# Performance work log

Hardware: AMD Instinct MI355X
Metric: run time of the kernel (lower is better)

## Reference

```python
import jax, jax.numpy as jnp
import numpy as np

E, TOPK, H, I, NSH = 8, 2, 2048, 5120, 2
B, S = 2, 1024


def setup_inputs() -> dict:
    key = jax.random.key(0)
    ks = jax.random.split(key, 8)
    sc = 0.02
    return {
        "x": jax.random.normal(ks[0], (B, S, H), dtype=jnp.float32),
        "w_router": jax.random.normal(ks[1], (E, H), dtype=jnp.float32),
        "wg": jax.random.normal(ks[2], (E, I, H), dtype=jnp.float32) * sc,
        "wu": jax.random.normal(ks[3], (E, I, H), dtype=jnp.float32) * sc,
        "wd": jax.random.normal(ks[4], (E, H, I), dtype=jnp.float32) * sc,
        "sg": jax.random.normal(ks[5], (NSH, I, H), dtype=jnp.float32) * sc,
        "su": jax.random.normal(ks[6], (NSH, I, H), dtype=jnp.float32) * sc,
        "sd": jax.random.normal(ks[7], (NSH, H, I), dtype=jnp.float32) * sc,
    }


def reference(x, w_router, wg, wu, wd, sg, su, sd):
    b, s, h = x.shape
    xt = x.reshape(-1, h)  # [T, H]
    T = xt.shape[0]

    # Router: fp32 linear, sigmoid scores, top-k, renormalize
    logits = jnp.einsum('th,eh->te', xt.astype(jnp.float32), w_router.astype(jnp.float32))
    scores = jax.nn.sigmoid(logits)
    topk_w, topk_i = jax.lax.top_k(scores, TOPK)
    topk_w = topk_w / jnp.sum(topk_w, axis=-1, keepdims=True)

    # Dense combine weights [T, E]: zero for non-selected experts
    comb = jnp.zeros((T, E), dtype=xt.dtype)
    comb = comb.at[jnp.arange(T)[:, None], topk_i].add(topk_w.astype(xt.dtype))

    # Routed experts (SwiGLU, no bias): compute all, combine with sparse weights
    gate = jax.nn.silu(jnp.einsum('th,eih->tei', xt, wg))
    up = jnp.einsum('th,eih->tei', xt, wu)
    expert_out = jnp.einsum('tei,ehi->teh', gate * up, wd)
    out = jnp.einsum('te,teh->th', comb, expert_out)

    # Shared experts: applied to every token, summed
    sgate = jax.nn.silu(jnp.einsum('th,jih->tji', xt, sg))
    sup = jnp.einsum('th,jih->tji', xt, su)
    out = out + jnp.einsum('tji,jhi->th', sgate * sup, sd)

    return out.reshape(b, s, h)
```

## Files before the change

kernel.cpp:

```cpp
#include <hip/hip_runtime.h>
#include <stdint.h>


#define E_ 8
#define H_ 2048
#define I_ 5120
#define T_ 2048
#define NSLOT 10

typedef __attribute__((ext_vector_type(4))) float f32x4;
typedef __attribute__((ext_vector_type(8))) __bf16 bf16x8;
typedef __attribute__((ext_vector_type(4))) unsigned int u32x4;
typedef __attribute__((ext_vector_type(2))) unsigned int u32x2;

__device__ __forceinline__ int sw(int r) { return (r ^ (r >> 2)) & 3; }

__device__ __forceinline__ unsigned short f2bf(float f) {
  unsigned u = __builtin_bit_cast(unsigned, f);
  u += 0x7FFFu + ((u >> 16) & 1u);
  return (unsigned short)(u >> 16);
}

__device__ __forceinline__ u32x2 cvt4(f32x4 v) {
  unsigned r0, r1;
  asm("v_cvt_pk_bf16_f32 %0, %1, %2" : "=v"(r0) : "v"(v[0]), "v"(v[1]));
  asm("v_cvt_pk_bf16_f32 %0, %1, %2" : "=v"(r1) : "v"(v[2]), "v"(v[3]));
  u32x2 w; w[0] = r0; w[1] = r1;
  return w;
}

__global__ __launch_bounds__(256) void k_castx(const float* __restrict__ x,
                                               unsigned short* __restrict__ xb) {
  const int i = (blockIdx.x * 256 + threadIdx.x) * 8;
  f32x4 a = *(const f32x4*)(x + i);
  f32x4 b = *(const f32x4*)(x + i + 4);
  u32x2 lo = cvt4(a), hi = cvt4(b);
  u32x4 o; o[0] = lo[0]; o[1] = lo[1]; o[2] = hi[0]; o[3] = hi[1];
  *(u32x4*)(xb + i) = o;
}

__global__ __launch_bounds__(64) void k_router(const float* __restrict__ x,
                                               const float* __restrict__ wr,
                                               int* __restrict__ tki,
                                               float* __restrict__ tkw) {
  const int t = blockIdx.x, lane = threadIdx.x;
  const float* xr = x + (size_t)t * H_;
  float lg[E_];
#pragma unroll
  for (int e = 0; e < E_; ++e) {
    const float* w = wr + (size_t)e * H_;
    float acc = 0.f;
    for (int k = lane; k < H_; k += 64) acc += xr[k] * w[k];
#pragma unroll
    for (int off = 32; off > 0; off >>= 1) acc += __shfl_down(acc, off);
    lg[e] = acc;
  }
  if (lane == 0) {
    float sc[E_];
#pragma unroll
    for (int e = 0; e < E_; ++e) sc[e] = 1.f / (1.f + expf(-lg[e]));
    int b0 = 0;
#pragma unroll
    for (int e = 1; e < E_; ++e) if (sc[e] > sc[b0]) b0 = e;
    int b1 = -1;
#pragma unroll
    for (int e = 0; e < E_; ++e) {
      if (e == b0) continue;
      if (b1 < 0 || sc[e] > sc[b1]) b1 = e;
    }
    float s0 = sc[b0], s1 = sc[b1], inv = 1.f / (s0 + s1);
    tki[2 * t] = b0; tki[2 * t + 1] = b1;
    tkw[2 * t] = s0 * inv; tkw[2 * t + 1] = s1 * inv;
  }
}

__global__ __launch_bounds__(64) void k_lists(const int* __restrict__ tki,
                                              const float* __restrict__ tkw,
                                              int* __restrict__ elist,
                                              float* __restrict__ ew,
                                              int* __restrict__ ecnt,
                                              int* __restrict__ ipos) {
  const int s = blockIdx.x, lane = threadIdx.x;
  if (s < E_) {
    int base = 0;
    for (int c = 0; c < T_ / 64; ++c) {
      int t = c * 64 + lane;
      int i0 = tki[2 * t], i1 = tki[2 * t + 1];
      int flag = (i0 == s) ? 1 : ((i1 == s) ? 2 : 0);
      unsigned long long m = __ballot(flag != 0);
      int pre = __popcll(m & ((1ull << lane) - 1ull));
      if (flag) {
        elist[s * T_ + base + pre] = t;
        ew[s * T_ + base + pre] = tkw[2 * t + flag - 1];
        ipos[2 * t + flag - 1] = base + pre;
      }
      base += __popcll(m);
    }
    int padded = (base + 255) & ~255;
    for (int p = base + lane; p < padded; p += 64) { elist[s * T_ + p] = 0; ew[s * T_ + p] = 0.f; }
    if (lane == 0) ecnt[s] = base;
  } else {
    for (int i = lane; i < T_; i += 64) { elist[s * T_ + i] = i; ew[s * T_ + i] = 1.f; }
    if (lane == 0) ecnt[s] = T_;
  }
}

__global__ void k_bases(const int* __restrict__ ecnt, int* __restrict__ sbase) {
  if (threadIdx.x == 0 && blockIdx.x == 0) {
    int b = 0;
    for (int s = 0; s < NSLOT; ++s) { sbase[s] = b; b += (ecnt[s] + 255) & ~255; }
  }
}

__global__ __launch_bounds__(1024, 4) void k_gateup(
    const unsigned short* __restrict__ xb,
    const float* __restrict__ wg_all, const float* __restrict__ wu_all,
    const float* __restrict__ sg_all, const float* __restrict__ su_all,
    const int* __restrict__ elist, const float* __restrict__ ew,
    const int* __restrict__ ecnt,
    const int* __restrict__ sbase, unsigned short* __restrict__ h) {
  const int s = blockIdx.z;
  const int cnt = ecnt[s];
  const int r0 = blockIdx.y * 256;
  if (r0 >= cnt) return;
  const int n0 = blockIdx.x * 128;
  const float* gw; const float* uw;
  if (s < E_) { gw = wg_all + (size_t)s * I_ * H_; uw = wu_all + (size_t)s * I_ * H_; }
  else        { gw = sg_all + (size_t)(s - E_) * I_ * H_; uw = su_all + (size_t)(s - E_) * I_ * H_; }
  const int* lst = elist + s * T_;
  const int hrow0 = sbase[s] + r0;

  __shared__ u32x4 sA[2][256 * 4];
  __shared__ u32x4 sG[2][128 * 4];
  __shared__ u32x4 sU[2][128 * 4];

  const int tid = threadIdx.x;
  const int w = tid >> 6, lane = tid & 63;
  const int wr = w >> 2, wc = w & 3;
  const int fr = lane & 15, k8 = lane >> 4;

  const int ar = tid >> 2, ca = tid & 3;
  int li = r0 + ar; if (li >= cnt) li = r0;
  const unsigned short* xp = xb + (size_t)lst[li] * H_ + ca * 8;
  const int br = tid >> 3, cb = (tid & 7) >> 1, bh = tid & 1;
  const float* gp = gw + (size_t)(n0 + br) * H_ + (tid & 7) * 4;
  const float* up = uw + (size_t)(n0 + br) * H_ + (tid & 7) * 4;

  u32x4 ra; f32x4 rg, ru;

  f32x4 accg[4][2], accu[4][2];
#pragma unroll
  for (int m = 0; m < 4; ++m)
#pragma unroll
    for (int n = 0; n < 2; ++n) {
      accg[m][n] = (f32x4){0.f, 0.f, 0.f, 0.f};
      accu[m][n] = (f32x4){0.f, 0.f, 0.f, 0.f};
    }

  auto loadNext = [&]() {
    ra = *(const u32x4*)xp; rg = *(const f32x4*)gp; ru = *(const f32x4*)up;
    xp += 32; gp += 32; up += 32;
  };
  auto stage = [&](int b) {
    sA[b][ar * 4 + (ca ^ sw(ar))] = ra;
    ((u32x2*)&sG[b][br * 4 + (cb ^ sw(br))])[bh] = cvt4(rg);
    ((u32x2*)&sU[b][br * 4 + (cb ^ sw(br))])[bh] = cvt4(ru);
  };
  auto compute = [&](int b) {
    bf16x8 af[4], gf[2], uf[2];
#pragma unroll
    for (int m = 0; m < 4; ++m) {
      int r = wr * 64 + m * 16 + fr;
      af[m] = __builtin_bit_cast(bf16x8, sA[b][r * 4 + (k8 ^ sw(r))]);
    }
#pragma unroll
    for (int n = 0; n < 2; ++n) {
      int r = wc * 32 + n * 16 + fr;
      gf[n] = __builtin_bit_cast(bf16x8, sG[b][r * 4 + (k8 ^ sw(r))]);
      uf[n] = __builtin_bit_cast(bf16x8, sU[b][r * 4 + (k8 ^ sw(r))]);
    }
#pragma unroll
    for (int m = 0; m < 4; ++m)
#pragma unroll
      for (int n = 0; n < 2; ++n) {
        accg[m][n] = __builtin_amdgcn_mfma_f32_16x16x32_bf16(af[m], gf[n], accg[m][n], 0, 0, 0);
        accu[m][n] = __builtin_amdgcn_mfma_f32_16x16x32_bf16(af[m], uf[n], accu[m][n], 0, 0, 0);
      }
  };

  const int KT = H_ / 32;
  loadNext();
  stage(0);
  loadNext();
  __syncthreads();
  int cur = 0;
  for (int kt = 0; kt < KT; ++kt) {
    compute(cur);
    if (kt + 1 < KT) {
      stage(cur ^ 1);
      if (kt + 2 < KT) loadNext();
      __syncthreads();
      cur ^= 1;
    }
  }

#pragma unroll
  for (int m = 0; m < 4; ++m)
#pragma unroll
    for (int r = 0; r < 4; ++r) {
      int rit = wr * 64 + m * 16 + k8 * 4 + r;
      if (r0 + rit < cnt) {
        float wgt = ew[s * T_ + r0 + rit];
        unsigned short* hrow = h + (size_t)(hrow0 + rit) * I_ + n0 + wc * 32;
#pragma unroll
        for (int n = 0; n < 2; ++n) {
          float g = accg[m][n][r], uv = accu[m][n][r];
          float hv = g / (1.f + expf(-g)) * uv * wgt;
          hrow[n * 16 + fr] = f2bf(hv);
        }
      }
    }
}

__global__ __launch_bounds__(512, 4) void k_down(
    const unsigned short* __restrict__ h,
    const float* __restrict__ wd_all, const float* __restrict__ sd_all,
    const int* __restrict__ elist,
    const int* __restrict__ ecnt, const int* __restrict__ sbase,
    float* __restrict__ y, int use_y,
    float* __restrict__ out) {
  const int s = blockIdx.z;
  const int cnt = ecnt[s];
  const int r0 = blockIdx.y * 256;
  if (r0 >= cnt) return;
  const int n0 = blockIdx.x * 128;
  const float* bw = (s < E_) ? wd_all + (size_t)s * H_ * I_
                             : sd_all + (size_t)(s - E_) * H_ * I_;
  const int hrow0 = sbase[s] + r0;

  __shared__ u32x4 sA[2][256 * 4];
  __shared__ u32x4 sB[2][128 * 4];

  const int tid = threadIdx.x;
  const int wv = tid >> 6, lane = tid & 63;
  const int wr = wv >> 1, wc = wv & 1;
  const int fr = lane & 15, k8 = lane >> 4;

  const int ar = tid >> 1, ca2 = (tid & 1) * 2;
  const unsigned short* hp = h + (size_t)(hrow0 + ar) * I_ + ca2 * 8;
  const int brr = tid >> 2, cb = tid & 3;
  const float* bp = bw + (size_t)(n0 + brr) * I_ + cb * 8;

  u32x4 ra0, ra1; f32x4 rb0, rb1;

  f32x4 acc[4][4];
#pragma unroll
  for (int m = 0; m < 4; ++m)
#pragma unroll
    for (int n = 0; n < 4; ++n) acc[m][n] = (f32x4){0.f, 0.f, 0.f, 0.f};

  auto loadNext = [&]() {
    ra0 = *(const u32x4*)hp; ra1 = *(const u32x4*)(hp + 8); hp += 32;
    rb0 = *(const f32x4*)bp; rb1 = *(const f32x4*)(bp + 4); bp += 32;
  };
  auto stage = [&](int b) {
    sA[b][ar * 4 + (ca2 ^ sw(ar))] = ra0;
    sA[b][ar * 4 + ((ca2 + 1) ^ sw(ar))] = ra1;
    u32x2 lo = cvt4(rb0), hi = cvt4(rb1);
    u32x4 q; q[0] = lo[0]; q[1] = lo[1]; q[2] = hi[0]; q[3] = hi[1];
    sB[b][brr * 4 + (cb ^ sw(brr))] = q;
  };
  auto compute = [&](int b) {
    bf16x8 af[4], bf[4];
#pragma unroll
    for (int m = 0; m < 4; ++m) {
      int r = wr * 64 + m * 16 + fr;
      af[m] = __builtin_bit_cast(bf16x8, sA[b][r * 4 + (k8 ^ sw(r))]);
    }
#pragma unroll
    for (int n = 0; n < 4; ++n) {
      int r = wc * 64 + n * 16 + fr;
      bf[n] = __builtin_bit_cast(bf16x8, sB[b][r * 4 + (k8 ^ sw(r))]);
    }
#pragma unroll
    for (int m = 0; m < 4; ++m)
#pragma unroll
      for (int n = 0; n < 4; ++n)
        acc[m][n] = __builtin_amdgcn_mfma_f32_16x16x32_bf16(af[m], bf[n], acc[m][n], 0, 0, 0);
  };

  const int KT = I_ / 32;
  loadNext();
  stage(0);
  loadNext();
  __syncthreads();
  int cur = 0;
  for (int kt = 0; kt < KT; ++kt) {
    compute(cur);
    if (kt + 1 < KT) {
      stage(cur ^ 1);
      if (kt + 2 < KT) loadNext();
      __syncthreads();
      cur ^= 1;
    }
  }

  if (use_y) {
#pragma unroll
    for (int m = 0; m < 4; ++m)
#pragma unroll
      for (int r = 0; r < 4; ++r) {
        int rit = wr * 64 + m * 16 + k8 * 4 + r;
        float* yrow = y + (size_t)(hrow0 + rit) * H_ + n0 + wc * 64 + fr;
#pragma unroll
        for (int n = 0; n < 4; ++n) yrow[n * 16] = acc[m][n][r];
      }
  } else {
    const int* lst = elist + s * T_;
#pragma unroll
    for (int m = 0; m < 4; ++m)
#pragma unroll
      for (int r = 0; r < 4; ++r) {
        int rit = wr * 64 + m * 16 + k8 * 4 + r;
        if (r0 + rit < cnt) {
          int t = lst[r0 + rit];
          float* orow = out + (size_t)t * H_ + n0 + wc * 64 + fr;
#pragma unroll
          for (int n = 0; n < 4; ++n) atomicAdd(orow + n * 16, acc[m][n][r]);
        }
      }
  }
}

__global__ __launch_bounds__(256) void k_combine(
    const float* __restrict__ y, const int* __restrict__ tki,
    const int* __restrict__ ipos, const int* __restrict__ sbase,
    float* __restrict__ out) {
  const int t = blockIdx.x;
  const int c = threadIdx.x * 8;
  const size_t r0 = (size_t)(sbase[tki[2 * t]] + ipos[2 * t]) * H_ + c;
  const size_t r1 = (size_t)(sbase[tki[2 * t + 1]] + ipos[2 * t + 1]) * H_ + c;
  const size_t r2 = (size_t)(sbase[8] + t) * H_ + c;
  const size_t r3 = (size_t)(sbase[9] + t) * H_ + c;
  f32x4 a0 = *(const f32x4*)(y + r0), b0 = *(const f32x4*)(y + r0 + 4);
  f32x4 a1 = *(const f32x4*)(y + r1), b1 = *(const f32x4*)(y + r1 + 4);
  f32x4 a2 = *(const f32x4*)(y + r2), b2 = *(const f32x4*)(y + r2 + 4);
  f32x4 a3 = *(const f32x4*)(y + r3), b3 = *(const f32x4*)(y + r3 + 4);
  f32x4 sa = (a0 + a1) + (a2 + a3);
  f32x4 sb = (b0 + b1) + (b2 + b3);
  float* o = out + (size_t)t * H_ + c;
  *(f32x4*)o = sa;
  *(f32x4*)(o + 4) = sb;
}

extern "C" void kernel_launch(void* const* d_in, const int* in_sizes, int n_in,
                              void* d_out, int out_size, void* d_ws, size_t ws_size,
                              hipStream_t stream) {
  const float* x  = (const float*)d_in[0];
  const float* wr = (const float*)d_in[1];
  const float* wg = (const float*)d_in[2];
  const float* wu = (const float*)d_in[3];
  const float* wd = (const float*)d_in[4];
  const float* sg = (const float*)d_in[5];
  const float* su = (const float*)d_in[6];
  const float* sd = (const float*)d_in[7];
  float* out = (float*)d_out;
  char* ws = (char*)d_ws;

  int*   tki   = (int*)(ws);
  float* tkw   = (float*)(ws + 16384);
  int*   elist = (int*)(ws + 32768);
  float* ew    = (float*)(ws + 114688);
  int*   ecnt  = (int*)(ws + 196608);
  int*   sbase = (int*)(ws + 196864);
  int*   ipos  = (int*)(ws + 197632);
  unsigned short* xb = (unsigned short*)(ws + 262144);
  unsigned short* h  = (unsigned short*)(ws + 262144 + 8388608);
  float* y = (float*)(ws + 262144 + 8388608 + 107479040);
  const size_t ws_need_y = 262144ull + 8388608ull + 107479040ull + 85983232ull;
  const int use_y = (ws_size >= ws_need_y) ? 1 : 0;

  k_castx<<<T_ * H_ / (256 * 8), 256, 0, stream>>>(x, xb);
  k_router<<<T_, 64, 0, stream>>>(x, wr, tki, tkw);
  k_lists<<<NSLOT, 64, 0, stream>>>(tki, tkw, elist, ew, ecnt, ipos);
  k_bases<<<1, 1, 0, stream>>>(ecnt, sbase);
  k_gateup<<<dim3(I_ / 128, T_ / 256, NSLOT), 1024, 0, stream>>>(
      xb, wg, wu, sg, su, elist, ew, ecnt, sbase, h);
  if (!use_y) hipMemsetAsync(out, 0, (size_t)T_ * H_ * sizeof(float), stream);
  k_down<<<dim3(H_ / 128, T_ / 256, NSLOT), 512, 0, stream>>>(
      h, wd, sd, elist, ecnt, sbase, y, use_y, out);
  if (use_y)
    k_combine<<<T_, 256, 0, stream>>>(y, tki, ipos, sbase, out);
}
```

Measured before the change: 998.7 us.

## Load bf16 activation tiles directly into LDS with a triple-buffered pipeline

Both GEMM kernels now fetch the already-bf16 A tiles (tokens for gate/up, hidden for down) with global_load_lds instead of staging them through registers. The source address is pre-swizzled so the LDS layout matches the existing XOR swizzle. A gets a three-slot ring buffer and waits use explicit vmcnt counts, so the next DMA stays in flight across the barrier. This aims to cut register pressure and VALU/LDS store work, at the cost of more LDS and fragile hand-counted waitcnt logic.

```diff
diff --git a/kernel.cpp b/kernel.cpp
--- a/kernel.cpp
+++ b/kernel.cpp
@@ -14,6 +14,20 @@
 typedef __attribute__((ext_vector_type(2))) unsigned int u32x2;
 
 __device__ __forceinline__ int sw(int r) { return (r ^ (r >> 2)) & 3; }
+
+typedef __attribute__((address_space(1))) const void* gptr1_t;
+typedef __attribute__((address_space(3))) void* lptr3_t;
+__device__ __forceinline__ void load_lds16(const void* g, void* l) {
+  __builtin_amdgcn_global_load_lds((gptr1_t)g, (lptr3_t)l, 16, 0, 0);
+}
+
+#define PIPE_SYNC(N)                                                    \
+  do {                                                                  \
+    asm volatile("s_waitcnt vmcnt(" #N ") lgkmcnt(0)" ::: "memory");    \
+    __builtin_amdgcn_sched_barrier(0);                                  \
+    __builtin_amdgcn_s_barrier();                                       \
+    __builtin_amdgcn_sched_barrier(0);                                  \
+  } while (0)
 
 __device__ __forceinline__ unsigned short f2bf(float f) {
   unsigned u = __builtin_bit_cast(unsigned, f);
@@ -130,23 +144,24 @@
   const int* lst = elist + s * T_;
   const int hrow0 = sbase[s] + r0;
 
-  __shared__ u32x4 sA[2][256 * 4];
-  __shared__ u32x4 sG[2][128 * 4];
-  __shared__ u32x4 sU[2][128 * 4];
+  __shared__ u32x4 sA[3][1024];
+  __shared__ u32x4 sG[2][512];
+  __shared__ u32x4 sU[2][512];
 
   const int tid = threadIdx.x;
-  const int w = tid >> 6, lane = tid & 63;
-  const int wr = w >> 2, wc = w & 3;
+  const int wv = tid >> 6, lane = tid & 63;
+  const int wr = wv >> 2, wc = wv & 3;
   const int fr = lane & 15, k8 = lane >> 4;
 
-  const int ar = tid >> 2, ca = tid & 3;
-  int li = r0 + ar; if (li >= cnt) li = r0;
-  const unsigned short* xp = xb + (size_t)lst[li] * H_ + ca * 8;
+  const int arow = wv * 16 + (lane >> 2);
+  int li = r0 + arow; if (li >= cnt) li = r0;
+  const unsigned short* aSrc =
+      xb + (size_t)lst[li] * H_ + (((lane & 3) ^ sw(arow)) * 8);
+
   const int br = tid >> 3, cb = (tid & 7) >> 1, bh = tid & 1;
   const float* gp = gw + (size_t)(n0 + br) * H_ + (tid & 7) * 4;
   const float* up = uw + (size_t)(n0 + br) * H_ + (tid & 7) * 4;
-
-  u32x4 ra; f32x4 rg, ru;
+  f32x4 rg, ru;
 
   f32x4 accg[4][2], accu[4][2];
 #pragma unroll
@@ -157,21 +172,23 @@
       accu[m][n] = (f32x4){0.f, 0.f, 0.f, 0.f};
     }
 
-  auto loadNext = [&]() {
-    ra = *(const u32x4*)xp; rg = *(const f32x4*)gp; ru = *(const f32x4*)up;
-    xp += 32; gp += 32; up += 32;
-  };
-  auto stage = [&](int b) {
-    sA[b][ar * 4 + (ca ^ sw(ar))] = ra;
+  auto dmaA = [&](int b, int kt) {
+    load_lds16(aSrc + kt * 32, &sA[b][wv * 64]);
+  };
+  auto loadB = [&]() {
+    rg = *(const f32x4*)gp; ru = *(const f32x4*)up;
+    gp += 32; up += 32;
+  };
+  auto stageB = [&](int b) {
     ((u32x2*)&sG[b][br * 4 + (cb ^ sw(br))])[bh] = cvt4(rg);
     ((u32x2*)&sU[b][br * 4 + (cb ^ sw(br))])[bh] = cvt4(ru);
   };
-  auto compute = [&](int b) {
+  auto compute = [&](int a, int b) {
     bf16x8 af[4], gf[2], uf[2];
 #pragma unroll
     for (int m = 0; m < 4; ++m) {
       int r = wr * 64 + m * 16 + fr;
-      af[m] = __builtin_bit_cast(bf16x8, sA[b][r * 4 + (k8 ^ sw(r))]);
+      af[m] = __builtin_bit_cast(bf16x8, sA[a][r * 4 + (k8 ^ sw(r))]);
     }
 #pragma unroll
     for (int n = 0; n < 2; ++n) {
@@ -189,18 +206,27 @@
   };
 
   const int KT = H_ / 32;
-  loadNext();
-  stage(0);
-  loadNext();
-  __syncthreads();
-  int cur = 0;
+  loadB();
+  dmaA(0, 0);
+  stageB(0);
+  loadB();
+  dmaA(1, 1);
+  PIPE_SYNC(3);
+  int aCur = 0, bCur = 0;
   for (int kt = 0; kt < KT; ++kt) {
-    compute(cur);
+    compute(aCur, bCur);
     if (kt + 1 < KT) {
-      stage(cur ^ 1);
-      if (kt + 2 < KT) loadNext();
-      __syncthreads();
-      cur ^= 1;
+      stageB(bCur ^ 1);
+      if (kt + 2 < KT) {
+        int nx = aCur + 2; if (nx >= 3) nx -= 3;
+        dmaA(nx, kt + 2);
+        loadB();
+        PIPE_SYNC(3);
+      } else {
+        PIPE_SYNC(0);
+      }
+      aCur = (aCur == 2) ? 0 : aCur + 1;
+      bCur ^= 1;
     }
   }
 
@@ -238,20 +264,24 @@
                              : sd_all + (size_t)(s - E_) * H_ * I_;
   const int hrow0 = sbase[s] + r0;
 
-  __shared__ u32x4 sA[2][256 * 4];
-  __shared__ u32x4 sB[2][128 * 4];
+  __shared__ u32x4 sA[3][1024];
+  __shared__ u32x4 sB[2][512];
 
   const int tid = threadIdx.x;
   const int wv = tid >> 6, lane = tid & 63;
   const int wr = wv >> 1, wc = wv & 1;
   const int fr = lane & 15, k8 = lane >> 4;
 
-  const int ar = tid >> 1, ca2 = (tid & 1) * 2;
-  const unsigned short* hp = h + (size_t)(hrow0 + ar) * I_ + ca2 * 8;
+  const int arow0 = wv * 32 + (lane >> 2);
+  const int arow1 = arow0 + 16;
+  const unsigned short* aSrc0 =
+      h + (size_t)(hrow0 + arow0) * I_ + (((lane & 3) ^ sw(arow0)) * 8);
+  const unsigned short* aSrc1 =
+      h + (size_t)(hrow0 + arow1) * I_ + (((lane & 3) ^ sw(arow1)) * 8);
+
   const int brr = tid >> 2, cb = tid & 3;
   const float* bp = bw + (size_t)(n0 + brr) * I_ + cb * 8;
-
-  u32x4 ra0, ra1; f32x4 rb0, rb1;
+  f32x4 rb0, rb1;
 
   f32x4 acc[4][4];
 #pragma unroll
@@ -259,23 +289,24 @@
 #pragma unroll
     for (int n = 0; n < 4; ++n) acc[m][n] = (f32x4){0.f, 0.f, 0.f, 0.f};
 
-  auto loadNext = [&]() {
-    ra0 = *(const u32x4*)hp; ra1 = *(const u32x4*)(hp + 8); hp += 32;
+  auto dmaA = [&](int b, int kt) {
+    load_lds16(aSrc0 + kt * 32, &sA[b][wv * 128]);
+    load_lds16(aSrc1 + kt * 32, &sA[b][wv * 128 + 64]);
+  };
+  auto loadB = [&]() {
     rb0 = *(const f32x4*)bp; rb1 = *(const f32x4*)(bp + 4); bp += 32;
   };
-  auto stage = [&](int b) {
-    sA[b][ar * 4 + (ca2 ^ sw(ar))] = ra0;
-    sA[b][ar * 4 + ((ca2 + 1) ^ sw(ar))] = ra1;
+  auto stageB = [&](int b) {
     u32x2 lo = cvt4(rb0), hi = cvt4(rb1);
     u32x4 q; q[0] = lo[0]; q[1] = lo[1]; q[2] = hi[0]; q[3] = hi[1];
     sB[b][brr * 4 + (cb ^ sw(brr))] = q;
   };
-  auto compute = [&](int b) {
+  auto compute = [&](int a, int b) {
     bf16x8 af[4], bf[4];
 #pragma unroll
     for (int m = 0; m < 4; ++m) {
       int r = wr * 64 + m * 16 + fr;
-      af[m] = __builtin_bit_cast(bf16x8, sA[b][r * 4 + (k8 ^ sw(r))]);
+      af[m] = __builtin_bit_cast(bf16x8, sA[a][r * 4 + (k8 ^ sw(r))]);
     }
 #pragma unroll
     for (int n = 0; n < 4; ++n) {
@@ -290,18 +321,27 @@
   };
 
   const int KT = I_ / 32;
-  loadNext();
-  stage(0);
-  loadNext();
-  __syncthreads();
-  int cur = 0;
+  loadB();
+  dmaA(0, 0);
+  stageB(0);
+  loadB();
+  dmaA(1, 1);
+  PIPE_SYNC(4);
+  int aCur = 0, bCur = 0;
   for (int kt = 0; kt < KT; ++kt) {
-    compute(cur);
+    compute(aCur, bCur);
     if (kt + 1 < KT) {
-      stage(cur ^ 1);
-      if (kt + 2 < KT) loadNext();
-      __syncthreads();
-      cur ^= 1;
+      stageB(bCur ^ 1);
+      if (kt + 2 < KT) {
+        int nx = aCur + 2; if (nx >= 3) nx -= 3;
+        dmaA(nx, kt + 2);
+        loadB();
+        PIPE_SYNC(4);
+      } else {
+        PIPE_SYNC(0);
+      }
+      aCur = (aCur == 2) ? 0 : aCur + 1;
+      bCur ^= 1;
     }
   }
 
```

Result: faster. 969.5 us (-2.9%).
